# Optimization experiments

Hardware: AMD Instinct MI355X
Metric: run time of the kernel (lower is better)

The kernel has to match this reference:

```python
import jax, jax.numpy as jnp
import numpy as np

B, N, D = 8, 4096, 64
NPOINT, NSAMPLE, RADIUS = 1024, 32, 0.2
MLP = [64, 64, 128]
IN_CH = 3 + D
EPS = 1e-5  # BatchNorm eps (torch default)


def setup_inputs() -> dict:
    key = jax.random.key(0)
    ks = jax.random.split(key, 2 + len(MLP))
    inp = {
        "xyz": jax.random.uniform(ks[0], (B, N, 3), jnp.float32),   # points in unit cube
        "points": jax.random.normal(ks[1], (B, N, D), jnp.float32),  # per-point features
    }
    last = IN_CH
    for i, out in enumerate(MLP):
        inp[f"w{i}"] = jax.random.normal(ks[2 + i], (out, last), jnp.float32) * 0.05  # 1x1 conv weight
        inp[f"b{i}"] = jnp.zeros((out,), jnp.float32)   # conv bias
        inp[f"g{i}"] = jnp.ones((out,), jnp.float32)    # BN gamma
        inp[f"be{i}"] = jnp.zeros((out,), jnp.float32)  # BN beta
        inp[f"m{i}"] = jnp.zeros((out,), jnp.float32)   # BN running mean
        inp[f"v{i}"] = jnp.ones((out,), jnp.float32)    # BN running var
        last = out
    return inp


def _fps(xyz, npoint):
    # Iterative farthest point sampling (deterministic start at index 0).
    Bb, Nn, _ = xyz.shape
    def step(carry, _):
        dist, far = carry
        centroid = xyz[jnp.arange(Bb), far][:, None, :]            # [B,1,3]
        d = jnp.sum((xyz - centroid) ** 2, axis=-1)                # [B,N]
        dist = jnp.minimum(dist, d)
        nfar = jnp.argmax(dist, axis=-1).astype(jnp.int32)
        return (dist, nfar), far
    init = (jnp.full((Bb, Nn), 1e10, xyz.dtype), jnp.zeros((Bb,), jnp.int32))
    _, idx = jax.lax.scan(step, init, None, length=npoint)
    return idx.T                                                   # [B,npoint]


def _index(p, idx):
    # p: [B,N,C], idx: [B,...] -> [B,...,C]
    return jax.vmap(lambda a, i: a[i])(p, idx)


def _ball_query(xyz, new_xyz):
    # For each query center, take first NSAMPLE point indices within RADIUS,
    # padding with the first found index (exactly PointNet++ query_ball_point).
    Nn = xyz.shape[1]
    sqr = jnp.sum((new_xyz[:, :, None, :] - xyz[:, None, :, :]) ** 2, axis=-1)  # [B,S,N]
    gidx = jnp.where(sqr > RADIUS ** 2, Nn, jnp.arange(Nn)[None, None, :])
    gidx = jnp.sort(gidx, axis=-1)[:, :, :NSAMPLE]                 # [B,S,K]
    first = gidx[:, :, :1]
    return jnp.where(gidx == Nn, first, gidx)


def reference(xyz, points, w0, b0, g0, be0, m0, v0,
              w1, b1, g1, be1, m1, v1,
              w2, b2, g2, be2, m2, v2):
    fps_idx = _fps(xyz, NPOINT)
    new_xyz = _index(xyz, fps_idx)                                 # [B,S,3]
    gidx = _ball_query(xyz, new_xyz)                               # [B,S,K]
    grouped_xyz = _index(xyz, gidx) - new_xyz[:, :, None, :]       # local coords [B,S,K,3]
    grouped_pts = _index(points, gidx)                             # [B,S,K,D]
    x = jnp.concatenate([grouped_xyz, grouped_pts], axis=-1)       # [B,S,K,3+D]
    layers = ((w0, b0, g0, be0, m0, v0),
              (w1, b1, g1, be1, m1, v1),
              (w2, b2, g2, be2, m2, v2))
    for w, b, g, be, m, v in layers:
        x = jnp.einsum('bskc,oc->bsko', x, w) + b                  # 1x1 conv (pointwise MLP)
        x = g * (x - m) * jax.lax.rsqrt(v + EPS) + be              # BN (eval mode)
        x = jax.nn.relu(x)
    new_points = jnp.max(x, axis=2)                                # max over neighbors -> [B,S,Cout]
    return new_xyz, new_points
```

## Files before the change

### kernel.cpp

```cpp
#include <hip/hip_runtime.h>
#include <hip/hip_bf16.h>
#include <stdint.h>

#define BATCH   8
#define NPTS    4096
#define DCH     64
#define NPOINT  1024
#define NSAMPLE 32
#define NEWXYZ_FLOATS (BATCH * NPOINT * 3)

typedef float v2f __attribute__((ext_vector_type(2)));

__device__ __forceinline__ float sqdist_rn(float px, float py, float pz,
                                           float cx, float cy, float cz) {
    float dx = __fsub_rn(px, cx);
    float dy = __fsub_rn(py, cy);
    float dz = __fsub_rn(pz, cz);
    return __fadd_rn(__fadd_rn(__fmul_rn(dx, dx), __fmul_rn(dy, dy)), __fmul_rn(dz, dz));
}

__device__ __forceinline__ unsigned long long ullmax(unsigned long long a, unsigned long long b) {
    return a > b ? a : b;
}

__global__ void prep_kernel(const float* __restrict__ w0, const float* __restrict__ b0,
                            const float* __restrict__ g0, const float* __restrict__ be0,
                            const float* __restrict__ m0, const float* __restrict__ v0,
                            const float* __restrict__ w1, const float* __restrict__ b1,
                            const float* __restrict__ g1, const float* __restrict__ be1,
                            const float* __restrict__ m1, const float* __restrict__ v1,
                            const float* __restrict__ w2, const float* __restrict__ b2,
                            const float* __restrict__ g2, const float* __restrict__ be2,
                            const float* __restrict__ m2, const float* __restrict__ v2,
                            float* __restrict__ wT0, float* __restrict__ wT1,
                            float* __restrict__ wT2, float* __restrict__ st) {
    const int tid  = blockIdx.x * blockDim.x + threadIdx.x;
    const int nthr = gridDim.x * blockDim.x;
    for (int i = tid; i < 64 * 67; i += nthr) { int o = i / 67, c = i % 67; wT0[c * 64 + o] = w0[i]; }
    for (int i = tid; i < 64 * 64; i += nthr) { int o = i >> 6, c = i & 63; wT1[c * 64 + o] = w1[i]; }
    for (int i = tid; i < 128 * 64; i += nthr) { int o = i >> 6, c = i & 63; wT2[c * 128 + o] = w2[i]; }
    if (tid < 64) {
        float s = g0[tid] / sqrtf(v0[tid] + 1e-5f);
        st[tid] = s;
        st[64 + tid] = (b0[tid] - m0[tid]) * s + be0[tid];
        s = g1[tid] / sqrtf(v1[tid] + 1e-5f);
        st[128 + tid] = s;
        st[192 + tid] = (b1[tid] - m1[tid]) * s + be1[tid];
    }
    if (tid < 128) {
        float s = g2[tid] / sqrtf(v2[tid] + 1e-5f);
        st[256 + tid] = s;
        st[384 + tid] = (b2[tid] - m2[tid]) * s + be2[tid];
    }
}

__global__ __launch_bounds__(512) void fps_kernel(const float* __restrict__ xyz,
                                                  float* __restrict__ newxyz) {
    __shared__ float4 sxyz[NPTS];
    __shared__ __align__(16) unsigned long long wkey[2][8];
    const int b    = blockIdx.x;
    const int tid  = threadIdx.x;
    const int lane = tid & 63;
    const int wid  = tid >> 6;
    const float* xb = xyz + (size_t)b * NPTS * 3;

    v2f px[4], py[4], pz[4];
    float dd[8];
#pragma unroll
    for (int i = 0; i < 8; ++i) {
        const int j = tid + i * 512;
        const float x = xb[3 * j], y = xb[3 * j + 1], z = xb[3 * j + 2];
        sxyz[j] = make_float4(x, y, z, 0.f);
        px[i >> 1][i & 1] = x;
        py[i >> 1][i & 1] = y;
        pz[i >> 1][i & 1] = z;
        dd[i] = 1e10f;
    }
    __syncthreads();

    const float4 c0v = sxyz[0];
    float cx = c0v.x, cy = c0v.y, cz = c0v.z;
    if (tid == 0) {
        float* o = newxyz + (size_t)b * NPOINT * 3;
        o[0] = cx; o[1] = cy; o[2] = cz;
    }

    for (int t = 1; t < NPOINT; ++t) {
        const v2f ncx = {-cx, -cx}, ncy = {-cy, -cy}, ncz = {-cz, -cz};
#pragma unroll
        for (int k = 0; k < 4; ++k) {
            v2f dx, dy, dz, qx, qy, qz, s1, s2;
            asm("v_pk_add_f32 %0, %1, %2" : "=v"(dx) : "v"(px[k]), "v"(ncx));
            asm("v_pk_add_f32 %0, %1, %2" : "=v"(dy) : "v"(py[k]), "v"(ncy));
            asm("v_pk_add_f32 %0, %1, %2" : "=v"(dz) : "v"(pz[k]), "v"(ncz));
            asm("v_pk_mul_f32 %0, %1, %1" : "=v"(qx) : "v"(dx));
            asm("v_pk_mul_f32 %0, %1, %1" : "=v"(qy) : "v"(dy));
            asm("v_pk_mul_f32 %0, %1, %1" : "=v"(qz) : "v"(dz));
            asm("v_pk_add_f32 %0, %1, %2" : "=v"(s1) : "v"(qx), "v"(qy));
            asm("v_pk_add_f32 %0, %1, %2" : "=v"(s2) : "v"(s1), "v"(qz));
            dd[2 * k]     = fminf(dd[2 * k],     s2[0]);
            dd[2 * k + 1] = fminf(dd[2 * k + 1], s2[1]);
        }
        float m = fmaxf(fmaxf(fmaxf(dd[0], dd[1]), fmaxf(dd[2], dd[3])),
                        fmaxf(fmaxf(dd[4], dd[5]), fmaxf(dd[6], dd[7])));
        int mb = __float_as_int(m);
#define FPS_RED(CTRL)                                                              \
        {                                                                          \
            int t_ = __builtin_amdgcn_update_dpp(0, mb, CTRL, 0xF, 0xF, true);     \
            mb = __float_as_int(fmaxf(__int_as_float(mb), __int_as_float(t_)));    \
        }
        FPS_RED(0x111)
        FPS_RED(0x112)
        FPS_RED(0x114)
        FPS_RED(0x118)
        FPS_RED(0x142)
        FPS_RED(0x143)
#undef FPS_RED
        const unsigned Mb = (unsigned)__builtin_amdgcn_readlane(mb, 63);

        unsigned jw = 0xFFFFFFFFu;
#pragma unroll
        for (int i = 7; i >= 0; --i) {
            const unsigned long long msk = __ballot(__float_as_uint(dd[i]) == Mb);
            if (msk) jw = (unsigned)(i * 512 + (wid << 6)) + (unsigned)__builtin_ctzll(msk);
        }
        const unsigned long long key =
            ((unsigned long long)Mb << 32) | (unsigned long long)(0xFFFFFFFFu - jw);
        if (lane == 0) wkey[t & 1][wid] = key;
        __syncthreads();

        const ulonglong2* wk = (const ulonglong2*)(&wkey[t & 1][0]);
        const ulonglong2 p0 = wk[0], p1 = wk[1], p2 = wk[2], p3 = wk[3];
        const unsigned long long v =
            ullmax(ullmax(ullmax(p0.x, p0.y), ullmax(p1.x, p1.y)),
                   ullmax(ullmax(p2.x, p2.y), ullmax(p3.x, p3.y)));
        const unsigned widx = 0xFFFFFFFFu - (unsigned)(v & 0xFFFFFFFFull);
        const float4 c = sxyz[widx];
        cx = c.x; cy = c.y; cz = c.z;
        if (tid == 0) {
            float* o = newxyz + ((size_t)b * NPOINT + t) * 3;
            o[0] = cx; o[1] = cy; o[2] = cz;
        }
    }
}

__global__ __launch_bounds__(256) void ballq_kernel(const float* __restrict__ xyz,
                                                    const float* __restrict__ newxyz,
                                                    int* __restrict__ gidx) {
    __shared__ int g[4][NSAMPLE];
    const int lane = threadIdx.x & 63;
    const int w    = threadIdx.x >> 6;
    const int q    = blockIdx.x * 4 + w;
    const int b    = q >> 10;
    const float* xb = xyz + (size_t)b * NPTS * 3;
    const float* c  = newxyz + (size_t)q * 3;
    const float cx = c[0], cy = c[1], cz = c[2];
    const float r2 = 0.04f;

    int cnt = 0;
    for (int base = 0; base < NPTS; base += 64) {
        const int j = base + lane;
        const float d = sqdist_rn(xb[j * 3 + 0], xb[j * 3 + 1], xb[j * 3 + 2], cx, cy, cz);
        const bool keep = !(d > r2);
        const unsigned long long m = __ballot(keep);
        if (keep) {
            const int slot = cnt + __popcll(m & ((1ull << lane) - 1ull));
            if (slot < NSAMPLE) g[w][slot] = j;
        }
        cnt += (int)__popcll(m);
        if (cnt >= NSAMPLE) break;
    }
    __syncthreads();
    const int first = g[w][0];
    if (lane < NSAMPLE) {
        const int v = (lane < cnt) ? g[w][lane] : first;
        gidx[(size_t)q * NSAMPLE + lane] = v;
    }
}

__global__ __launch_bounds__(256) void mlp_kernel(
    const float* __restrict__ xyz, const float* __restrict__ points,
    const float* __restrict__ newxyz, const int* __restrict__ gidx,
    const float* __restrict__ wT0, const float* __restrict__ wT1,
    const float* __restrict__ wT2, const float* __restrict__ st,
    float* __restrict__ outp) {
    __shared__ float Xs[4][68][36];
    const int lane = threadIdx.x & 63;
    const int w    = threadIdx.x >> 6;
    const int q    = blockIdx.x * 4 + w;
    const int b    = q >> 10;
    float (*X)[36] = Xs[w];
    const int* gi = gidx + (size_t)q * NSAMPLE;
    const float* nc = newxyz + (size_t)q * 3;
    const float c0 = nc[0], c1 = nc[1], c2 = nc[2];

    for (int k = 0; k < NSAMPLE; ++k) {
        const int idx = gi[k];
        X[3 + lane][k] = points[((size_t)b * NPTS + idx) * DCH + lane];
        if (lane < 3) {
            const float cv = (lane == 0) ? c0 : ((lane == 1) ? c1 : c2);
            X[lane][k] = xyz[((size_t)b * NPTS + idx) * 3 + lane] - cv;
        }
    }

    const int kk = lane >> 3;
    const int oo = lane & 7;

    float acc[4][8];
#pragma unroll
    for (int i = 0; i < 4; ++i)
#pragma unroll
        for (int j = 0; j < 8; ++j) acc[i][j] = 0.f;

    for (int c = 0; c < 67; ++c) {
        const float4 xv = *reinterpret_cast<const float4*>(&X[c][4 * kk]);
        const float4 wa = *reinterpret_cast<const float4*>(&wT0[c * 64 + 8 * oo]);
        const float4 wb = *reinterpret_cast<const float4*>(&wT0[c * 64 + 8 * oo + 4]);
        const float xr[4] = {xv.x, xv.y, xv.z, xv.w};
        const float wr[8] = {wa.x, wa.y, wa.z, wa.w, wb.x, wb.y, wb.z, wb.w};
#pragma unroll
        for (int i = 0; i < 4; ++i)
#pragma unroll
            for (int j = 0; j < 8; ++j)
                acc[i][j] = fmaf(xr[i], wr[j], acc[i][j]);
    }
    {
        const float4 sa = *reinterpret_cast<const float4*>(&st[8 * oo]);
        const float4 sb = *reinterpret_cast<const float4*>(&st[8 * oo + 4]);
        const float4 ta = *reinterpret_cast<const float4*>(&st[64 + 8 * oo]);
        const float4 tb = *reinterpret_cast<const float4*>(&st[64 + 8 * oo + 4]);
        const float sr[8] = {sa.x, sa.y, sa.z, sa.w, sb.x, sb.y, sb.z, sb.w};
        const float tr[8] = {ta.x, ta.y, ta.z, ta.w, tb.x, tb.y, tb.z, tb.w};
#pragma unroll
        for (int j = 0; j < 8; ++j) {
            float4 v;
            v.x = fmaxf(fmaf(acc[0][j], sr[j], tr[j]), 0.f);
            v.y = fmaxf(fmaf(acc[1][j], sr[j], tr[j]), 0.f);
            v.z = fmaxf(fmaf(acc[2][j], sr[j], tr[j]), 0.f);
            v.w = fmaxf(fmaf(acc[3][j], sr[j], tr[j]), 0.f);
            *reinterpret_cast<float4*>(&X[8 * oo + j][4 * kk]) = v;
        }
    }

#pragma unroll
    for (int i = 0; i < 4; ++i)
#pragma unroll
        for (int j = 0; j < 8; ++j) acc[i][j] = 0.f;

    for (int c = 0; c < 64; ++c) {
        const float4 xv = *reinterpret_cast<const float4*>(&X[c][4 * kk]);
        const float4 wa = *reinterpret_cast<const float4*>(&wT1[c * 64 + 8 * oo]);
        const float4 wb = *reinterpret_cast<const float4*>(&wT1[c * 64 + 8 * oo + 4]);
        const float xr[4] = {xv.x, xv.y, xv.z, xv.w};
        const float wr[8] = {wa.x, wa.y, wa.z, wa.w, wb.x, wb.y, wb.z, wb.w};
#pragma unroll
        for (int i = 0; i < 4; ++i)
#pragma unroll
            for (int j = 0; j < 8; ++j)
                acc[i][j] = fmaf(xr[i], wr[j], acc[i][j]);
    }
    {
        const float4 sa = *reinterpret_cast<const float4*>(&st[128 + 8 * oo]);
        const float4 sb = *reinterpret_cast<const float4*>(&st[128 + 8 * oo + 4]);
        const float4 ta = *reinterpret_cast<const float4*>(&st[192 + 8 * oo]);
        const float4 tb = *reinterpret_cast<const float4*>(&st[192 + 8 * oo + 4]);
        const float sr[8] = {sa.x, sa.y, sa.z, sa.w, sb.x, sb.y, sb.z, sb.w};
        const float tr[8] = {ta.x, ta.y, ta.z, ta.w, tb.x, tb.y, tb.z, tb.w};
#pragma unroll
        for (int j = 0; j < 8; ++j) {
            float4 v;
            v.x = fmaxf(fmaf(acc[0][j], sr[j], tr[j]), 0.f);
            v.y = fmaxf(fmaf(acc[1][j], sr[j], tr[j]), 0.f);
            v.z = fmaxf(fmaf(acc[2][j], sr[j], tr[j]), 0.f);
            v.w = fmaxf(fmaf(acc[3][j], sr[j], tr[j]), 0.f);
            *reinterpret_cast<float4*>(&X[8 * oo + j][4 * kk]) = v;
        }
    }

    float a2[4][16];
#pragma unroll
    for (int i = 0; i < 4; ++i)
#pragma unroll
        for (int j = 0; j < 16; ++j) a2[i][j] = 0.f;

    for (int c = 0; c < 64; ++c) {
        const float4 xv = *reinterpret_cast<const float4*>(&X[c][4 * kk]);
        const float xr[4] = {xv.x, xv.y, xv.z, xv.w};
        float wr[16];
#pragma unroll
        for (int j4 = 0; j4 < 4; ++j4) {
            const float4 wv = *reinterpret_cast<const float4*>(&wT2[c * 128 + 16 * oo + 4 * j4]);
            wr[4 * j4 + 0] = wv.x; wr[4 * j4 + 1] = wv.y;
            wr[4 * j4 + 2] = wv.z; wr[4 * j4 + 3] = wv.w;
        }
#pragma unroll
        for (int i = 0; i < 4; ++i)
#pragma unroll
            for (int j = 0; j < 16; ++j)
                a2[i][j] = fmaf(xr[i], wr[j], a2[i][j]);
    }

    float mx[16];
#pragma unroll
    for (int j = 0; j < 16; ++j) {
        const float sj = st[256 + 16 * oo + j];
        const float tj = st[384 + 16 * oo + j];
        float mm = fmaxf(fmaf(a2[0][j], sj, tj), 0.f);
        mm = fmaxf(mm, fmaxf(fmaf(a2[1][j], sj, tj), 0.f));
        mm = fmaxf(mm, fmaxf(fmaf(a2[2][j], sj, tj), 0.f));
        mm = fmaxf(mm, fmaxf(fmaf(a2[3][j], sj, tj), 0.f));
        mx[j] = mm;
    }
#pragma unroll
    for (int j = 0; j < 16; ++j) {
        mx[j] = fmaxf(mx[j], __shfl_xor(mx[j], 8, 64));
        mx[j] = fmaxf(mx[j], __shfl_xor(mx[j], 16, 64));
        mx[j] = fmaxf(mx[j], __shfl_xor(mx[j], 32, 64));
    }
    if (kk == 0) {
        float* dst = outp + (size_t)q * 128 + 16 * oo;
#pragma unroll
        for (int j4 = 0; j4 < 4; ++j4) {
            float4 v;
            v.x = mx[4 * j4 + 0]; v.y = mx[4 * j4 + 1];
            v.z = mx[4 * j4 + 2]; v.w = mx[4 * j4 + 3];
            *reinterpret_cast<float4*>(&dst[4 * j4]) = v;
        }
    }
}

extern "C" void kernel_launch(void* const* d_in, const int* in_sizes, int n_in,
                              void* d_out, int out_size, void* d_ws, size_t ws_size,
                              hipStream_t stream) {
    const float* xyz    = (const float*)d_in[0];
    const float* points = (const float*)d_in[1];
    const float* w0  = (const float*)d_in[2];
    const float* b0  = (const float*)d_in[3];
    const float* g0  = (const float*)d_in[4];
    const float* be0 = (const float*)d_in[5];
    const float* m0  = (const float*)d_in[6];
    const float* v0  = (const float*)d_in[7];
    const float* w1  = (const float*)d_in[8];
    const float* b1  = (const float*)d_in[9];
    const float* g1  = (const float*)d_in[10];
    const float* be1 = (const float*)d_in[11];
    const float* m1  = (const float*)d_in[12];
    const float* v1  = (const float*)d_in[13];
    const float* w2  = (const float*)d_in[14];
    const float* b2  = (const float*)d_in[15];
    const float* g2  = (const float*)d_in[16];
    const float* be2 = (const float*)d_in[17];
    const float* m2  = (const float*)d_in[18];
    const float* v2  = (const float*)d_in[19];

    float* out = (float*)d_out;
    float* ws  = (float*)d_ws;
    float* wT0 = ws;
    float* wT1 = ws + 4288;
    float* wT2 = ws + 8384;
    float* st  = ws + 16576;
    int*   gidx = (int*)(ws + 17088);

    prep_kernel<<<dim3(17), dim3(256), 0, stream>>>(w0, b0, g0, be0, m0, v0,
                                                    w1, b1, g1, be1, m1, v1,
                                                    w2, b2, g2, be2, m2, v2,
                                                    wT0, wT1, wT2, st);
    fps_kernel<<<dim3(BATCH), dim3(512), 0, stream>>>(xyz, out);
    ballq_kernel<<<dim3(2048), dim3(256), 0, stream>>>(xyz, out, gidx);
    mlp_kernel<<<dim3(2048), dim3(256), 0, stream>>>(xyz, points, out, gidx,
                                                     wT0, wT1, wT2, st,
                                                     out + NEWXYZ_FLOATS);
}
```

Measured before the change: 1.032 ms.

## Interleave two batches per FPS block to overlap barrier latency

The FPS kernel now processes two batches per block with 256 threads (4 waves) instead of one batch with 512 threads. The two batches' iterations are staggered so that one batch's distance update and wave reduction overlaps the other's cross-wave combine, which removes one barrier per batch step. Each thread now holds 16 points per batch, so register pressure roughly quadruples. Only 4 blocks run, so fewer CUs are used and per-wave serial work grows.

```diff
diff --git a/kernel.cpp b/kernel.cpp
--- a/kernel.cpp
+++ b/kernel.cpp
@@ -54,93 +54,130 @@
     }
 }
 
-__global__ __launch_bounds__(512) void fps_kernel(const float* __restrict__ xyz,
-                                                  float* __restrict__ newxyz) {
-    __shared__ float4 sxyz[NPTS];
-    __shared__ __align__(16) unsigned long long wkey[2][8];
-    const int b    = blockIdx.x;
-    const int tid  = threadIdx.x;
-    const int lane = tid & 63;
-    const int wid  = tid >> 6;
-    const float* xb = xyz + (size_t)b * NPTS * 3;
-
-    v2f px[4], py[4], pz[4];
-    float dd[8];
-#pragma unroll
-    for (int i = 0; i < 8; ++i) {
-        const int j = tid + i * 512;
-        const float x = xb[3 * j], y = xb[3 * j + 1], z = xb[3 * j + 2];
-        sxyz[j] = make_float4(x, y, z, 0.f);
-        px[i >> 1][i & 1] = x;
-        py[i >> 1][i & 1] = y;
-        pz[i >> 1][i & 1] = z;
-        dd[i] = 1e10f;
-    }
-    __syncthreads();
-
-    const float4 c0v = sxyz[0];
-    float cx = c0v.x, cy = c0v.y, cz = c0v.z;
-    if (tid == 0) {
-        float* o = newxyz + (size_t)b * NPOINT * 3;
-        o[0] = cx; o[1] = cy; o[2] = cz;
-    }
-
-    for (int t = 1; t < NPOINT; ++t) {
-        const v2f ncx = {-cx, -cx}, ncy = {-cy, -cy}, ncz = {-cz, -cz};
-#pragma unroll
-        for (int k = 0; k < 4; ++k) {
-            v2f dx, dy, dz, qx, qy, qz, s1, s2;
-            asm("v_pk_add_f32 %0, %1, %2" : "=v"(dx) : "v"(px[k]), "v"(ncx));
-            asm("v_pk_add_f32 %0, %1, %2" : "=v"(dy) : "v"(py[k]), "v"(ncy));
-            asm("v_pk_add_f32 %0, %1, %2" : "=v"(dz) : "v"(pz[k]), "v"(ncz));
-            asm("v_pk_mul_f32 %0, %1, %1" : "=v"(qx) : "v"(dx));
-            asm("v_pk_mul_f32 %0, %1, %1" : "=v"(qy) : "v"(dy));
-            asm("v_pk_mul_f32 %0, %1, %1" : "=v"(qz) : "v"(dz));
-            asm("v_pk_add_f32 %0, %1, %2" : "=v"(s1) : "v"(qx), "v"(qy));
-            asm("v_pk_add_f32 %0, %1, %2" : "=v"(s2) : "v"(s1), "v"(qz));
-            dd[2 * k]     = fminf(dd[2 * k],     s2[0]);
-            dd[2 * k + 1] = fminf(dd[2 * k + 1], s2[1]);
-        }
-        float m = fmaxf(fmaxf(fmaxf(dd[0], dd[1]), fmaxf(dd[2], dd[3])),
-                        fmaxf(fmaxf(dd[4], dd[5]), fmaxf(dd[6], dd[7])));
-        int mb = __float_as_int(m);
 #define FPS_RED(CTRL)                                                              \
         {                                                                          \
             int t_ = __builtin_amdgcn_update_dpp(0, mb, CTRL, 0xF, 0xF, true);     \
             mb = __float_as_int(fmaxf(__int_as_float(mb), __int_as_float(t_)));    \
         }
-        FPS_RED(0x111)
-        FPS_RED(0x112)
-        FPS_RED(0x114)
-        FPS_RED(0x118)
-        FPS_RED(0x142)
-        FPS_RED(0x143)
-#undef FPS_RED
-        const unsigned Mb = (unsigned)__builtin_amdgcn_readlane(mb, 63);
-
-        unsigned jw = 0xFFFFFFFFu;
-#pragma unroll
-        for (int i = 7; i >= 0; --i) {
-            const unsigned long long msk = __ballot(__float_as_uint(dd[i]) == Mb);
-            if (msk) jw = (unsigned)(i * 512 + (wid << 6)) + (unsigned)__builtin_ctzll(msk);
-        }
-        const unsigned long long key =
-            ((unsigned long long)Mb << 32) | (unsigned long long)(0xFFFFFFFFu - jw);
-        if (lane == 0) wkey[t & 1][wid] = key;
+
+__device__ __forceinline__ void fps_phase(float (&dd)[16],
+                                          const v2f (&px)[8], const v2f (&py)[8],
+                                          const v2f (&pz)[8],
+                                          float cx, float cy, float cz,
+                                          unsigned long long* wkeyW,
+                                          int lane, int wid) {
+    const v2f ncx = {-cx, -cx}, ncy = {-cy, -cy}, ncz = {-cz, -cz};
+#pragma unroll
+    for (int k = 0; k < 8; ++k) {
+        v2f dx, dy, dz, qx, qy, qz, s1, s2;
+        asm("v_pk_add_f32 %0, %1, %2" : "=v"(dx) : "v"(px[k]), "v"(ncx));
+        asm("v_pk_add_f32 %0, %1, %2" : "=v"(dy) : "v"(py[k]), "v"(ncy));
+        asm("v_pk_add_f32 %0, %1, %2" : "=v"(dz) : "v"(pz[k]), "v"(ncz));
+        asm("v_pk_mul_f32 %0, %1, %1" : "=v"(qx) : "v"(dx));
+        asm("v_pk_mul_f32 %0, %1, %1" : "=v"(qy) : "v"(dy));
+        asm("v_pk_mul_f32 %0, %1, %1" : "=v"(qz) : "v"(dz));
+        asm("v_pk_add_f32 %0, %1, %2" : "=v"(s1) : "v"(qx), "v"(qy));
+        asm("v_pk_add_f32 %0, %1, %2" : "=v"(s2) : "v"(s1), "v"(qz));
+        dd[2 * k]     = fminf(dd[2 * k],     s2[0]);
+        dd[2 * k + 1] = fminf(dd[2 * k + 1], s2[1]);
+    }
+    float m = fmaxf(fmaxf(fmaxf(fmaxf(dd[0], dd[1]), fmaxf(dd[2], dd[3])),
+                          fmaxf(fmaxf(dd[4], dd[5]), fmaxf(dd[6], dd[7]))),
+                    fmaxf(fmaxf(fmaxf(dd[8], dd[9]), fmaxf(dd[10], dd[11])),
+                          fmaxf(fmaxf(dd[12], dd[13]), fmaxf(dd[14], dd[15]))));
+    int mb = __float_as_int(m);
+    FPS_RED(0x111)
+    FPS_RED(0x112)
+    FPS_RED(0x114)
+    FPS_RED(0x118)
+    FPS_RED(0x142)
+    FPS_RED(0x143)
+    const unsigned Mb = (unsigned)__builtin_amdgcn_readlane(mb, 63);
+    unsigned jw = 0xFFFFFFFFu;
+#pragma unroll
+    for (int i = 15; i >= 0; --i) {
+        const unsigned long long msk = __ballot(__float_as_uint(dd[i]) == Mb);
+        if (msk) jw = (unsigned)(i * 256 + (wid << 6)) + (unsigned)__builtin_ctzll(msk);
+    }
+    if (lane == 0)
+        wkeyW[wid] = ((unsigned long long)Mb << 32) | (unsigned long long)(0xFFFFFFFFu - jw);
+}
+
+__device__ __forceinline__ void fps_combine(const unsigned long long* wkeyR,
+                                            const float4* sxyz,
+                                            float& cx, float& cy, float& cz) {
+    const ulonglong2* wk = (const ulonglong2*)wkeyR;
+    const ulonglong2 a = wk[0], b = wk[1];
+    const unsigned long long v = ullmax(ullmax(a.x, a.y), ullmax(b.x, b.y));
+    const unsigned widx = 0xFFFFFFFFu - (unsigned)(v & 0xFFFFFFFFull);
+    const float4 c = sxyz[widx];
+    cx = c.x; cy = c.y; cz = c.z;
+}
+
+__global__ __launch_bounds__(256, 1) void fps_kernel(const float* __restrict__ xyz,
+                                                     float* __restrict__ newxyz) {
+    __shared__ float4 sxyzA[NPTS];
+    __shared__ float4 sxyzB[NPTS];
+    __shared__ __align__(16) unsigned long long wkeyA[2][4];
+    __shared__ __align__(16) unsigned long long wkeyB[2][4];
+    const int tid  = threadIdx.x;
+    const int lane = tid & 63;
+    const int wid  = tid >> 6;
+    const int bA   = 2 * blockIdx.x;
+    const int bB   = bA + 1;
+    const float* xbA = xyz + (size_t)bA * NPTS * 3;
+    const float* xbB = xyz + (size_t)bB * NPTS * 3;
+    float* outA = newxyz + (size_t)bA * NPOINT * 3;
+    float* outB = newxyz + (size_t)bB * NPOINT * 3;
+
+    v2f pxA[8], pyA[8], pzA[8], pxB[8], pyB[8], pzB[8];
+    float ddA[16], ddB[16];
+#pragma unroll
+    for (int i = 0; i < 16; ++i) {
+        const int p = tid + i * 256;
+        {
+            const float x = xbA[3 * p], y = xbA[3 * p + 1], z = xbA[3 * p + 2];
+            sxyzA[p] = make_float4(x, y, z, 0.f);
+            pxA[i >> 1][i & 1] = x; pyA[i >> 1][i & 1] = y; pzA[i >> 1][i & 1] = z;
+            ddA[i] = 1e10f;
+        }
+        {
+            const float x = xbB[3 * p], y = xbB[3 * p + 1], z = xbB[3 * p + 2];
+            sxyzB[p] = make_float4(x, y, z, 0.f);
+            pxB[i >> 1][i & 1] = x; pyB[i >> 1][i & 1] = y; pzB[i >> 1][i & 1] = z;
+            ddB[i] = 1e10f;
+        }
+    }
+    float cxA = xbA[0], cyA = xbA[1], czA = xbA[2];
+    float cxB = xbB[0], cyB = xbB[1], czB = xbB[2];
+    if (tid == 0) {
+        outA[0] = cxA; outA[1] = cyA; outA[2] = czA;
+        outB[0] = cxB; outB[1] = cyB; outB[2] = czB;
+    }
+    __syncthreads();
+
+    for (int t = 1; t < NPOINT; ++t) {
+        fps_phase(ddA, pxA, pyA, pzA, cxA, cyA, czA, &wkeyA[t & 1][0], lane, wid);
+        if (t > 1) {
+            fps_combine(&wkeyB[(t - 1) & 1][0], sxyzB, cxB, cyB, czB);
+            if (tid == 0) {
+                float* o = outB + (size_t)(t - 1) * 3;
+                o[0] = cxB; o[1] = cyB; o[2] = czB;
+            }
+        }
         __syncthreads();
-
-        const ulonglong2* wk = (const ulonglong2*)(&wkey[t & 1][0]);
-        const ulonglong2 p0 = wk[0], p1 = wk[1], p2 = wk[2], p3 = wk[3];
-        const unsigned long long v =
-            ullmax(ullmax(ullmax(p0.x, p0.y), ullmax(p1.x, p1.y)),
-                   ullmax(ullmax(p2.x, p2.y), ullmax(p3.x, p3.y)));
-        const unsigned widx = 0xFFFFFFFFu - (unsigned)(v & 0xFFFFFFFFull);
-        const float4 c = sxyz[widx];
-        cx = c.x; cy = c.y; cz = c.z;
+        fps_phase(ddB, pxB, pyB, pzB, cxB, cyB, czB, &wkeyB[t & 1][0], lane, wid);
+        fps_combine(&wkeyA[t & 1][0], sxyzA, cxA, cyA, czA);
         if (tid == 0) {
-            float* o = newxyz + ((size_t)b * NPOINT + t) * 3;
-            o[0] = cx; o[1] = cy; o[2] = cz;
-        }
+            float* o = outA + (size_t)t * 3;
+            o[0] = cxA; o[1] = cyA; o[2] = czA;
+        }
+        __syncthreads();
+    }
+    fps_combine(&wkeyB[(NPOINT - 1) & 1][0], sxyzB, cxB, cyB, czB);
+    if (tid == 0) {
+        float* o = outB + (size_t)(NPOINT - 1) * 3;
+        o[0] = cxB; o[1] = cyB; o[2] = czB;
     }
 }
 
@@ -365,7 +402,7 @@
                                                     w1, b1, g1, be1, m1, v1,
                                                     w2, b2, g2, be2, m2, v2,
                                                     wT0, wT1, wT2, st);
-    fps_kernel<<<dim3(BATCH), dim3(512), 0, stream>>>(xyz, out);
+    fps_kernel<<<dim3(BATCH / 2), dim3(256), 0, stream>>>(xyz, out);
     ballq_kernel<<<dim3(2048), dim3(256), 0, stream>>>(xyz, out, gidx);
     mlp_kernel<<<dim3(2048), dim3(256), 0, stream>>>(xyz, points, out, gidx,
                                                      wT0, wT1, wT2, st,
```

Result: slower. 1.899 ms (+84.0%).

## Reduce FPS argmax with packed 64-bit DPP keys and LDS atomicMax

Applied to the files above, without the earlier changes.

Each FPS step now packs the per-lane max distance and inverted index into one 64-bit key and reduces it across the wave with DPP. Lane 63 of each wave then does an LDS atomicMax into a triple-buffered slot, so there is one barrier per step and no per-element ballots or cross-wave key array. Separately, the layer-0/1 output channels are permuted in the transposed weights and BN tables, and the matching X store index changes, which looks aimed at LDS bank conflicts in the MLP kernel. The cost is twice as many DPP ops per reduction step, plus LDS atomics whose contention across the eight waves could add latency to the serial FPS loop.

```diff
diff --git a/kernel.cpp b/kernel.cpp
--- a/kernel.cpp
+++ b/kernel.cpp
@@ -21,6 +21,15 @@
 
 __device__ __forceinline__ unsigned long long ullmax(unsigned long long a, unsigned long long b) {
     return a > b ? a : b;
+}
+
+template <int CTRL>
+__device__ __forceinline__ unsigned long long dpp_u64(unsigned long long v) {
+    int lo = (int)(unsigned)(v & 0xFFFFFFFFull);
+    int hi = (int)(unsigned)(v >> 32);
+    lo = __builtin_amdgcn_update_dpp(0, lo, CTRL, 0xF, 0xF, true);
+    hi = __builtin_amdgcn_update_dpp(0, hi, CTRL, 0xF, 0xF, true);
+    return ((unsigned long long)(unsigned)hi << 32) | (unsigned)lo;
 }
 
 __global__ void prep_kernel(const float* __restrict__ w0, const float* __restrict__ b0,
@@ -36,16 +45,23 @@
                             float* __restrict__ wT2, float* __restrict__ st) {
     const int tid  = blockIdx.x * blockDim.x + threadIdx.x;
     const int nthr = gridDim.x * blockDim.x;
-    for (int i = tid; i < 64 * 67; i += nthr) { int o = i / 67, c = i % 67; wT0[c * 64 + o] = w0[i]; }
-    for (int i = tid; i < 64 * 64; i += nthr) { int o = i >> 6, c = i & 63; wT1[c * 64 + o] = w1[i]; }
+    for (int i = tid; i < 64 * 67; i += nthr) {
+        int o = i / 67, c = i % 67;
+        wT0[c * 64 + (((o & 7) << 3) | (o >> 3))] = w0[i];
+    }
+    for (int i = tid; i < 64 * 64; i += nthr) {
+        int o = i >> 6, c = i & 63;
+        wT1[c * 64 + (((o & 7) << 3) | (o >> 3))] = w1[i];
+    }
     for (int i = tid; i < 128 * 64; i += nthr) { int o = i >> 6, c = i & 63; wT2[c * 128 + o] = w2[i]; }
     if (tid < 64) {
+        const int col = ((tid & 7) << 3) | (tid >> 3);
         float s = g0[tid] / sqrtf(v0[tid] + 1e-5f);
-        st[tid] = s;
-        st[64 + tid] = (b0[tid] - m0[tid]) * s + be0[tid];
+        st[col] = s;
+        st[64 + col] = (b0[tid] - m0[tid]) * s + be0[tid];
         s = g1[tid] / sqrtf(v1[tid] + 1e-5f);
-        st[128 + tid] = s;
-        st[192 + tid] = (b1[tid] - m1[tid]) * s + be1[tid];
+        st[128 + col] = s;
+        st[192 + col] = (b1[tid] - m1[tid]) * s + be1[tid];
     }
     if (tid < 128) {
         float s = g2[tid] / sqrtf(v2[tid] + 1e-5f);
@@ -54,18 +70,18 @@
     }
 }
 
-__global__ __launch_bounds__(512) void fps_kernel(const float* __restrict__ xyz,
-                                                  float* __restrict__ newxyz) {
+__global__ __launch_bounds__(512, 1) void fps_kernel(const float* __restrict__ xyz,
+                                                     float* __restrict__ newxyz) {
     __shared__ float4 sxyz[NPTS];
-    __shared__ __align__(16) unsigned long long wkey[2][8];
+    __shared__ unsigned long long kbuf[3];
     const int b    = blockIdx.x;
     const int tid  = threadIdx.x;
     const int lane = tid & 63;
-    const int wid  = tid >> 6;
     const float* xb = xyz + (size_t)b * NPTS * 3;
 
     v2f px[4], py[4], pz[4];
     float dd[8];
+    unsigned invj[8];
 #pragma unroll
     for (int i = 0; i < 8; ++i) {
         const int j = tid + i * 512;
@@ -75,15 +91,16 @@
         py[i >> 1][i & 1] = y;
         pz[i >> 1][i & 1] = z;
         dd[i] = 1e10f;
-    }
-    __syncthreads();
-
-    const float4 c0v = sxyz[0];
-    float cx = c0v.x, cy = c0v.y, cz = c0v.z;
+        invj[i] = 0xFFFFFFFFu - (unsigned)j;
+    }
+    if (tid < 3) kbuf[tid] = 0ull;
+
+    float cx = xb[0], cy = xb[1], cz = xb[2];
     if (tid == 0) {
         float* o = newxyz + (size_t)b * NPOINT * 3;
         o[0] = cx; o[1] = cy; o[2] = cz;
     }
+    __syncthreads();
 
     for (int t = 1; t < NPOINT; ++t) {
         const v2f ncx = {-cx, -cx}, ncy = {-cy, -cy}, ncz = {-cz, -cz};
@@ -101,39 +118,25 @@
             dd[2 * k]     = fminf(dd[2 * k],     s2[0]);
             dd[2 * k + 1] = fminf(dd[2 * k + 1], s2[1]);
         }
-        float m = fmaxf(fmaxf(fmaxf(dd[0], dd[1]), fmaxf(dd[2], dd[3])),
-                        fmaxf(fmaxf(dd[4], dd[5]), fmaxf(dd[6], dd[7])));
-        int mb = __float_as_int(m);
-#define FPS_RED(CTRL)                                                              \
-        {                                                                          \
-            int t_ = __builtin_amdgcn_update_dpp(0, mb, CTRL, 0xF, 0xF, true);     \
-            mb = __float_as_int(fmaxf(__int_as_float(mb), __int_as_float(t_)));    \
-        }
-        FPS_RED(0x111)
-        FPS_RED(0x112)
-        FPS_RED(0x114)
-        FPS_RED(0x118)
-        FPS_RED(0x142)
-        FPS_RED(0x143)
-#undef FPS_RED
-        const unsigned Mb = (unsigned)__builtin_amdgcn_readlane(mb, 63);
-
-        unsigned jw = 0xFFFFFFFFu;
-#pragma unroll
-        for (int i = 7; i >= 0; --i) {
-            const unsigned long long msk = __ballot(__float_as_uint(dd[i]) == Mb);
-            if (msk) jw = (unsigned)(i * 512 + (wid << 6)) + (unsigned)__builtin_ctzll(msk);
-        }
-        const unsigned long long key =
-            ((unsigned long long)Mb << 32) | (unsigned long long)(0xFFFFFFFFu - jw);
-        if (lane == 0) wkey[t & 1][wid] = key;
+        const float m = fmaxf(fmaxf(fmaxf(dd[0], dd[1]), fmaxf(dd[2], dd[3])),
+                              fmaxf(fmaxf(dd[4], dd[5]), fmaxf(dd[6], dd[7])));
+        unsigned inv = invj[0];
+#pragma unroll
+        for (int i = 7; i >= 0; --i)
+            if (dd[i] == m) inv = invj[i];
+        unsigned long long key =
+            ((unsigned long long)__float_as_uint(m) << 32) | (unsigned long long)inv;
+        key = ullmax(key, dpp_u64<0x111>(key));
+        key = ullmax(key, dpp_u64<0x112>(key));
+        key = ullmax(key, dpp_u64<0x114>(key));
+        key = ullmax(key, dpp_u64<0x118>(key));
+        key = ullmax(key, dpp_u64<0x142>(key));
+        key = ullmax(key, dpp_u64<0x143>(key));
+        if (lane == 63) atomicMax(&kbuf[t % 3], key);
+        if (tid == 0) kbuf[(t + 1) % 3] = 0ull;
         __syncthreads();
 
-        const ulonglong2* wk = (const ulonglong2*)(&wkey[t & 1][0]);
-        const ulonglong2 p0 = wk[0], p1 = wk[1], p2 = wk[2], p3 = wk[3];
-        const unsigned long long v =
-            ullmax(ullmax(ullmax(p0.x, p0.y), ullmax(p1.x, p1.y)),
-                   ullmax(ullmax(p2.x, p2.y), ullmax(p3.x, p3.y)));
+        const unsigned long long v = kbuf[t % 3];
         const unsigned widx = 0xFFFFFFFFu - (unsigned)(v & 0xFFFFFFFFull);
         const float4 c = sxyz[widx];
         cx = c.x; cy = c.y; cz = c.z;
@@ -238,7 +241,7 @@
             v.y = fmaxf(fmaf(acc[1][j], sr[j], tr[j]), 0.f);
             v.z = fmaxf(fmaf(acc[2][j], sr[j], tr[j]), 0.f);
             v.w = fmaxf(fmaf(acc[3][j], sr[j], tr[j]), 0.f);
-            *reinterpret_cast<float4*>(&X[8 * oo + j][4 * kk]) = v;
+            *reinterpret_cast<float4*>(&X[oo + 8 * j][4 * kk]) = v;
         }
     }
 
@@ -273,7 +276,7 @@
             v.y = fmaxf(fmaf(acc[1][j], sr[j], tr[j]), 0.f);
             v.z = fmaxf(fmaf(acc[2][j], sr[j], tr[j]), 0.f);
             v.w = fmaxf(fmaf(acc[3][j], sr[j], tr[j]), 0.f);
-            *reinterpret_cast<float4*>(&X[8 * oo + j][4 * kk]) = v;
+            *reinterpret_cast<float4*>(&X[oo + 8 * j][4 * kk]) = v;
         }
     }
 
```

After: 1.030 ms. No clear change (-0.2%).
